# Optimization experiments

Hardware: AMD Instinct MI355X
Metric: run time of the kernel (lower is better)

Reference implementation:

```python
import jax, jax.numpy as jnp
import numpy as np

B_BOX, N_CLASS = 2, 20          # B, C from __init__
LAMBDA_C, LAMBDA_N = 5.0, 0.5   # self.lambda_c, self.lambda_n
GRID = 49                        # hard-coded 7x7 grid


def setup_inputs() -> dict:
    key = jax.random.key(0)
    k1, k2 = jax.random.split(key)
    outputs = jax.random.uniform(k1, (16384, GRID, 5 * B_BOX + N_CLASS), dtype=jnp.float32)
    target = jax.random.uniform(k2, (16384, 10, 5), dtype=jnp.float32)
    return {"outputs": outputs, "target": target}


def _forward(outputs, target):
    batch, n_obj = target.shape[0], target.shape[1]
    Bb = B_BOX
    # --- target preprocessing: sqrt(w,h), nan -> -1 ---
    tgt = target.at[:, :, 2:4].set(jnp.sqrt(target[:, :, 2:4]))
    tgt = jnp.nan_to_num(tgt, nan=-1.0)
    # --- grid-cell assignment (vectorized version of the batch*obj python loop) ---
    x, y = tgt[:, :, 0], tgt[:, :, 1]
    xi = jnp.trunc(7.0 * x).astype(jnp.int32)   # int(7*x) truncation semantics
    yi = jnp.trunc(7.0 * y).astype(jnp.int32)
    cell = jnp.clip(7 * yi + xi, 0, GRID - 1)
    valid = ((x != -1.0) & (xi >= 0)).astype(tgt.dtype)
    sel = jax.nn.one_hot(cell, GRID, dtype=tgt.dtype) * valid[..., None]   # [b,obj,49]
    ti = sel[:, :, :, None] * tgt[:, :, None, :]                           # [b,obj,49,5]
    ti = jnp.transpose(ti, (0, 2, 1, 3))                                   # [b,49,obj,5]
    # --- permute: move first Bb nonzero boxes of each cell to the top ---
    nonzero = jnp.sum(ti, axis=-1) > 0                                     # [b,49,obj]
    slot = jnp.cumsum(nonzero.astype(jnp.int32), axis=-1) - 1
    slot = jnp.where(nonzero, jnp.minimum(slot, Bb), Bb)                   # Bb = discard slot
    oh = jax.nn.one_hot(slot, Bb + 1, dtype=ti.dtype)                      # [b,49,obj,Bb+1]
    gt = jnp.einsum('bcos,bcod->bcsd', oh, ti)[:, :, :Bb]                  # [b,49,Bb,5]
    # --- iou_matrix (boxes stored as center +/- (sqrt_wh)^2 corners) ---
    pred5 = outputs[:, :, :5 * Bb].reshape(batch, GRID, Bb, 5)
    pdims = pred5[..., :4]
    pdims = pdims.at[..., 2:4].set(jnp.sqrt(pdims[..., 2:4]))
    gdims = gt[..., :4]
    gmin, gmax = gdims[..., :2] - gdims[..., 2:4] ** 2, gdims[..., :2] + gdims[..., 2:4] ** 2
    pmin, pmax = pdims[..., :2] - pdims[..., 2:4] ** 2, pdims[..., :2] + pdims[..., 2:4] ** 2
    # pairwise: axis2 = pred box, axis3 = gt box
    imin = jnp.maximum(gmin[:, :, None, :, :], pmin[:, :, :, None, :])
    imax = jnp.minimum(gmax[:, :, None, :, :], pmax[:, :, :, None, :])
    d = jnp.maximum(imax - imin, 0.0)
    inter = d[..., 0] * d[..., 1]                                          # [b,49,Bb,Bb]
    gwh, pwh = jnp.abs(gmax - gmin), jnp.abs(pmax - pmin)
    garea = (gwh[..., 0] * gwh[..., 1])[:, :, None, :]
    parea = (pwh[..., 0] * pwh[..., 1])[:, :, :, None]
    union = garea + parea - inter
    iou = jnp.where(union == 0, 0.0, inter / jnp.where(union == 0, 1.0, union))  # nan_to_num(i/u)
    t_index = jnp.argmax(iou, axis=2)                                      # [b,49,Bb]
    # --- construct_model_ground_truth: gather assigned gt box + truncated-int confidence ---
    idx = jnp.broadcast_to(t_index[..., None], gt.shape)
    gathered = jnp.take_along_axis(gt, idx, axis=2)                        # [b,49,Bb,5]
    r1wh, r2wh = pred5[..., 2:4] ** 2, gathered[..., 2:4] ** 2
    min1, max1 = pred5[..., :2] - 0.5 * r1wh, pred5[..., :2] + 0.5 * r1wh
    min2, max2 = gathered[..., :2] - 0.5 * r2wh, gathered[..., :2] + 0.5 * r2wh
    d2 = jnp.maximum(jnp.minimum(max1, max2) - jnp.maximum(min1, min2), 0.0)
    inter2 = d2[..., 0] * d2[..., 1]
    union2 = r1wh[..., 0] * r1wh[..., 1] + r2wh[..., 0] * r2wh[..., 1] - inter2
    conf = jnp.where((jnp.trunc(union2) == 0) | (jnp.trunc(inter2) == 0), 0.0,
                     jnp.trunc(inter2 / jnp.where(union2 == 0, 1.0, union2)))
    final_gt = gathered.at[..., 4].set(conf)
    # --- obj loss: lambda_c on x,y,w,h; 1.0 on confidence ---
    w = jnp.array([LAMBDA_C, LAMBDA_C, LAMBDA_C, LAMBDA_C, 1.0], dtype=outputs.dtype)
    obj_loss = jnp.sum(w * (final_gt - pred5) ** 2)
    # --- noobj loss (faithfully replicates original bug: mask is recreated per loop
    #     iteration, so only the last (batch, bbox) iteration's mask survives) ---
    pconf, gconf = pred5[..., 4], final_gt[..., 4]                         # [b,49,Bb]
    mask = jnp.ones_like(gconf)
    mask = mask.at[batch - 1, jnp.arange(GRID), t_index[batch - 1, :, Bb - 1]].set(0.0)
    noobj_loss = LAMBDA_N * jnp.sum(((pconf - gconf) * mask) ** 2)
    # --- class loss ---
    cls_scores = outputs[:, :, 5 * Bb:]                                    # [b,49,C]
    max_pred = jnp.max(cls_scores, axis=2)[..., None]                      # [b,49,1]
    pred_cls = jnp.argmax(cls_scores, axis=2)[..., None]                   # [b,49,1]
    predictions = max_pred * pconf                                         # [b,49,Bb]
    truths = (final_gt[..., 4] == pred_cls.astype(outputs.dtype)).astype(outputs.dtype)
    cell_mask = jnp.sign(jnp.sum(final_gt, axis=-1))                       # [b,49,Bb]
    class_loss = jnp.sum(cell_mask * (truths - predictions) ** 2)
    return (obj_loss + noobj_loss + class_loss) / batch


def reference(outputs, target):
    return _forward(outputs, target)
```

## Files before the change

### kernel.cpp

```cpp
#include <hip/hip_runtime.h>
#include <math.h>

#define GRID_CELLS 49
#define NOBJ 10
#define BB 2
#define NCLS 20
#define OUT_C 30
#define LAMBDA_C 5.0f
#define LAMBDA_N 0.5f
#define BLOCK 256

__global__ __launch_bounds__(BLOCK, 4) void yolo_loss_flat(
    const float* __restrict__ outputs,
    const float* __restrict__ target,
    float* __restrict__ out,
    int batch, float inv_batch)
{
    const int gid = blockIdx.x * BLOCK + threadIdx.x;
    float lsum = 0.0f;

    if (gid < batch * GRID_CELLS) {
        const int b = gid / GRID_CELLS;
        const int c = gid - b * GRID_CELLS;

        float g0[5] = {0.f, 0.f, 0.f, 0.f, 0.f};
        float g1[5] = {0.f, 0.f, 0.f, 0.f, 0.f};
        int cnt = 0;
        const float2* t2 = reinterpret_cast<const float2*>(target + (size_t)b * (NOBJ * 5));
        #pragma unroll
        for (int i = 0; i < 5; ++i) {
            float2 a0 = t2[5 * i + 0];
            float2 a1 = t2[5 * i + 1];
            float2 a2 = t2[5 * i + 2];
            float2 a3 = t2[5 * i + 3];
            float2 a4 = t2[5 * i + 4];
            float v[10] = {a0.x, a0.y, a1.x, a1.y, a2.x, a2.y, a3.x, a3.y, a4.x, a4.y};
            #pragma unroll
            for (int h = 0; h < 2; ++h) {
                float t0 = v[5 * h + 0];
                float t1 = v[5 * h + 1];
                float t2f = sqrtf(v[5 * h + 2]);
                float t3f = sqrtf(v[5 * h + 3]);
                float t4 = v[5 * h + 4];
                if (t0 != t0)  t0  = -1.0f;
                if (t1 != t1)  t1  = -1.0f;
                if (t2f != t2f) t2f = -1.0f;
                if (t3f != t3f) t3f = -1.0f;
                if (t4 != t4)  t4  = -1.0f;
                int xi = (int)truncf(7.0f * t0);
                int yi = (int)truncf(7.0f * t1);
                int cell = 7 * yi + xi;
                cell = cell < 0 ? 0 : (cell > GRID_CELLS - 1 ? GRID_CELLS - 1 : cell);
                bool valid = (t0 != -1.0f) && (xi >= 0);
                float s5 = t0 + t1 + t2f + t3f + t4;
                if (valid && (s5 > 0.0f) && cell == c) {
                    if (cnt == 0)      { g0[0]=t0; g0[1]=t1; g0[2]=t2f; g0[3]=t3f; g0[4]=t4; }
                    else if (cnt == 1) { g1[0]=t0; g1[1]=t1; g1[2]=t2f; g1[3]=t3f; g1[4]=t4; }
                    ++cnt;
                }
            }
        }
        float g[BB][5];
        #pragma unroll
        for (int d = 0; d < 5; ++d) { g[0][d] = g0[d]; g[1][d] = g1[d]; }

        const float2* r2 = reinterpret_cast<const float2*>(outputs + (size_t)gid * OUT_C);
        float pred[BB][5];
        {
            float2 p0 = r2[0], p1 = r2[1], p2 = r2[2], p3 = r2[3], p4 = r2[4];
            pred[0][0] = p0.x; pred[0][1] = p0.y; pred[0][2] = p1.x; pred[0][3] = p1.y; pred[0][4] = p2.x;
            pred[1][0] = p2.y; pred[1][1] = p3.x; pred[1][2] = p3.y; pred[1][3] = p4.x; pred[1][4] = p4.y;
        }
        float maxp; int cls;
        {
            float2 q0 = r2[5];
            maxp = q0.x; cls = 0;
            if (q0.y > maxp) { maxp = q0.y; cls = 1; }
            #pragma unroll
            for (int i = 1; i < NCLS / 2; ++i) {
                float2 q = r2[5 + i];
                if (q.x > maxp) { maxp = q.x; cls = 2 * i; }
                if (q.y > maxp) { maxp = q.y; cls = 2 * i + 1; }
            }
        }
        float fcls = (float)cls;

        float pminx[BB], pmaxx[BB], pminy[BB], pmaxy[BB], parea[BB];
        #pragma unroll
        for (int p = 0; p < BB; ++p) {
            float sw = sqrtf(pred[p][2]);
            float sh = sqrtf(pred[p][3]);
            float w2 = sw * sw, h2 = sh * sh;
            pminx[p] = pred[p][0] - w2; pmaxx[p] = pred[p][0] + w2;
            pminy[p] = pred[p][1] - h2; pmaxy[p] = pred[p][1] + h2;
            parea[p] = fabsf(pmaxx[p] - pminx[p]) * fabsf(pmaxy[p] - pminy[p]);
        }
        float gminx[BB], gmaxx[BB], gminy[BB], gmaxy[BB], garea[BB];
        #pragma unroll
        for (int s = 0; s < BB; ++s) {
            float w2 = g[s][2] * g[s][2], h2 = g[s][3] * g[s][3];
            gminx[s] = g[s][0] - w2; gmaxx[s] = g[s][0] + w2;
            gminy[s] = g[s][1] - h2; gmaxy[s] = g[s][1] + h2;
            garea[s] = fabsf(gmaxx[s] - gminx[s]) * fabsf(gmaxy[s] - gminy[s]);
        }
        int t_index[BB];
        #pragma unroll
        for (int s = 0; s < BB; ++s) {
            float best = 0.0f; int bi = 0;
            #pragma unroll
            for (int p = 0; p < BB; ++p) {
                float ix0 = fmaxf(gminx[s], pminx[p]);
                float iy0 = fmaxf(gminy[s], pminy[p]);
                float ix1 = fminf(gmaxx[s], pmaxx[p]);
                float iy1 = fminf(gmaxy[s], pmaxy[p]);
                float dx = fmaxf(ix1 - ix0, 0.0f);
                float dy = fmaxf(iy1 - iy0, 0.0f);
                float inter = dx * dy;
                float uni = garea[s] + parea[p] - inter;
                float iou = (uni == 0.0f) ? 0.0f : inter / uni;
                if (p == 0) { best = iou; bi = 0; }
                else if (iou > best) { best = iou; bi = p; }
            }
            t_index[s] = bi;
        }

        #pragma unroll
        for (int s = 0; s < BB; ++s) {
            float ga[5];
            #pragma unroll
            for (int d = 0; d < 5; ++d) ga[d] = (t_index[s] == 0) ? g[0][d] : g[1][d];
            float r1w = pred[s][2] * pred[s][2], r1h = pred[s][3] * pred[s][3];
            float r2w = ga[2] * ga[2],           r2h = ga[3] * ga[3];
            float min1x = pred[s][0] - 0.5f * r1w, max1x = pred[s][0] + 0.5f * r1w;
            float min1y = pred[s][1] - 0.5f * r1h, max1y = pred[s][1] + 0.5f * r1h;
            float min2x = ga[0] - 0.5f * r2w, max2x = ga[0] + 0.5f * r2w;
            float min2y = ga[1] - 0.5f * r2h, max2y = ga[1] + 0.5f * r2h;
            float dx = fmaxf(fminf(max1x, max2x) - fmaxf(min1x, min2x), 0.0f);
            float dy = fmaxf(fminf(max1y, max2y) - fmaxf(min1y, min2y), 0.0f);
            float inter2 = dx * dy;
            float uni2 = r1w * r1h + r2w * r2h - inter2;
            float conf;
            if (truncf(uni2) == 0.0f || truncf(inter2) == 0.0f) conf = 0.0f;
            else conf = truncf(inter2 / (uni2 == 0.0f ? 1.0f : uni2));
            #pragma unroll
            for (int d = 0; d < 4; ++d) {
                float df = ga[d] - pred[s][d];
                lsum += LAMBDA_C * df * df;
            }
            { float df = conf - pred[s][4]; lsum += df * df; }
            float m = 1.0f;
            if (b == batch - 1 && s == t_index[BB - 1]) m = 0.0f;
            float dn = (pred[s][4] - conf) * m;
            lsum += LAMBDA_N * dn * dn;
            float predn = maxp * pred[s][4];
            float truth = (conf == fcls) ? 1.0f : 0.0f;
            float sum5 = ga[0] + ga[1] + ga[2] + ga[3] + conf;
            float cm = (sum5 > 0.0f) ? 1.0f : ((sum5 < 0.0f) ? -1.0f : 0.0f);
            float dcl = truth - predn;
            lsum += cm * dcl * dcl;
        }
    }

    #pragma unroll
    for (int off = 32; off > 0; off >>= 1) lsum += __shfl_down(lsum, off, 64);
    __shared__ float red[BLOCK / 64];
    const int wid = threadIdx.x >> 6;
    const int lane = threadIdx.x & 63;
    if (lane == 0) red[wid] = lsum;
    __syncthreads();
    if (threadIdx.x == 0) {
        float s = 0.0f;
        #pragma unroll
        for (int w = 0; w < BLOCK / 64; ++w) s += red[w];
        atomicAdd(out, s * inv_batch);
    }
}

extern "C" void kernel_launch(void* const* d_in, const int* in_sizes, int n_in,
                              void* d_out, int out_size, void* d_ws, size_t ws_size,
                              hipStream_t stream) {
    const float* outputs = (const float*)d_in[0];
    const float* target  = (const float*)d_in[1];
    float* out = (float*)d_out;
    int batch = in_sizes[1] / (NOBJ * 5);
    int total = batch * GRID_CELLS;
    int nblocks = (total + BLOCK - 1) / BLOCK;
    hipMemsetAsync(out, 0, sizeof(float), stream);
    yolo_loss_flat<<<nblocks, BLOCK, 0, stream>>>(outputs, target, out, batch, 1.0f / (float)batch);
}
```

Measured before the change: 158.6 us.

## Scatter targets into shared-memory cell grid per block instead of per-thread scans

Each block now handles 5 whole batch items. Target objects are preprocessed once per object and scattered into a shared-memory per-cell ground-truth table, instead of every cell thread re-reading and re-testing all 10 targets. This removes redundant target loads and per-cell preprocessing. In exchange it adds two barriers, about 11KB of shared memory per block and a grid-wide zeroing pass. Only 245 of 256 threads do cell work, and the launch_bounds occupancy hint is dropped.

```diff
diff --git a/kernel.cpp b/kernel.cpp
--- a/kernel.cpp
+++ b/kernel.cpp
@@ -9,61 +9,84 @@
 #define LAMBDA_C 5.0f
 #define LAMBDA_N 0.5f
 #define BLOCK 256
-
-__global__ __launch_bounds__(BLOCK, 4) void yolo_loss_flat(
+#define ITEMS 5
+#define CELLW 11
+
+__global__ __launch_bounds__(BLOCK) void yolo_loss_shared(
     const float* __restrict__ outputs,
     const float* __restrict__ target,
     float* __restrict__ out,
     int batch, float inv_batch)
 {
-    const int gid = blockIdx.x * BLOCK + threadIdx.x;
+    __shared__ int   cellA[ITEMS][NOBJ];
+    __shared__ int   nzA[ITEMS][NOBJ];
+    __shared__ float tval[ITEMS][NOBJ][5];
+    __shared__ float gt[ITEMS][GRID_CELLS][CELLW];
+    __shared__ float red[BLOCK / 64];
+
+    const int t = threadIdx.x;
+    const int b0 = blockIdx.x * ITEMS;
+
+    for (int i = t; i < ITEMS * GRID_CELLS * CELLW; i += BLOCK)
+        (&gt[0][0][0])[i] = 0.0f;
+
+    if (t < ITEMS * NOBJ) {
+        const int li = t / NOBJ;
+        const int o  = t - li * NOBJ;
+        const int b  = b0 + li;
+        if (b < batch) {
+            const float* tp = target + (size_t)b * (NOBJ * 5) + o * 5;
+            float t0 = tp[0], t1 = tp[1];
+            float t2f = sqrtf(tp[2]), t3f = sqrtf(tp[3]);
+            float t4 = tp[4];
+            if (t0 != t0)   t0  = -1.0f;
+            if (t1 != t1)   t1  = -1.0f;
+            if (t2f != t2f) t2f = -1.0f;
+            if (t3f != t3f) t3f = -1.0f;
+            if (t4 != t4)   t4  = -1.0f;
+            int xi = (int)truncf(7.0f * t0);
+            int yi = (int)truncf(7.0f * t1);
+            int cell = 7 * yi + xi;
+            cell = cell < 0 ? 0 : (cell > GRID_CELLS - 1 ? GRID_CELLS - 1 : cell);
+            bool valid = (t0 != -1.0f) && (xi >= 0);
+            float s5 = t0 + t1 + t2f + t3f + t4;
+            cellA[li][o] = cell;
+            nzA[li][o] = (valid && (s5 > 0.0f)) ? 1 : 0;
+            tval[li][o][0] = t0; tval[li][o][1] = t1; tval[li][o][2] = t2f;
+            tval[li][o][3] = t3f; tval[li][o][4] = t4;
+        } else {
+            nzA[li][o] = 0;
+        }
+    }
+    __syncthreads();
+
+    if (t < ITEMS * NOBJ) {
+        const int li = t / NOBJ;
+        const int o  = t - li * NOBJ;
+        if (nzA[li][o]) {
+            const int c = cellA[li][o];
+            int slot = 0;
+            for (int p = 0; p < o; ++p) slot += (nzA[li][p] && cellA[li][p] == c) ? 1 : 0;
+            if (slot < BB) {
+                #pragma unroll
+                for (int d = 0; d < 5; ++d) gt[li][c][slot * 5 + d] = tval[li][o][d];
+            }
+        }
+    }
+    __syncthreads();
+
     float lsum = 0.0f;
-
-    if (gid < batch * GRID_CELLS) {
-        const int b = gid / GRID_CELLS;
-        const int c = gid - b * GRID_CELLS;
-
-        float g0[5] = {0.f, 0.f, 0.f, 0.f, 0.f};
-        float g1[5] = {0.f, 0.f, 0.f, 0.f, 0.f};
-        int cnt = 0;
-        const float2* t2 = reinterpret_cast<const float2*>(target + (size_t)b * (NOBJ * 5));
-        #pragma unroll
-        for (int i = 0; i < 5; ++i) {
-            float2 a0 = t2[5 * i + 0];
-            float2 a1 = t2[5 * i + 1];
-            float2 a2 = t2[5 * i + 2];
-            float2 a3 = t2[5 * i + 3];
-            float2 a4 = t2[5 * i + 4];
-            float v[10] = {a0.x, a0.y, a1.x, a1.y, a2.x, a2.y, a3.x, a3.y, a4.x, a4.y};
-            #pragma unroll
-            for (int h = 0; h < 2; ++h) {
-                float t0 = v[5 * h + 0];
-                float t1 = v[5 * h + 1];
-                float t2f = sqrtf(v[5 * h + 2]);
-                float t3f = sqrtf(v[5 * h + 3]);
-                float t4 = v[5 * h + 4];
-                if (t0 != t0)  t0  = -1.0f;
-                if (t1 != t1)  t1  = -1.0f;
-                if (t2f != t2f) t2f = -1.0f;
-                if (t3f != t3f) t3f = -1.0f;
-                if (t4 != t4)  t4  = -1.0f;
-                int xi = (int)truncf(7.0f * t0);
-                int yi = (int)truncf(7.0f * t1);
-                int cell = 7 * yi + xi;
-                cell = cell < 0 ? 0 : (cell > GRID_CELLS - 1 ? GRID_CELLS - 1 : cell);
-                bool valid = (t0 != -1.0f) && (xi >= 0);
-                float s5 = t0 + t1 + t2f + t3f + t4;
-                if (valid && (s5 > 0.0f) && cell == c) {
-                    if (cnt == 0)      { g0[0]=t0; g0[1]=t1; g0[2]=t2f; g0[3]=t3f; g0[4]=t4; }
-                    else if (cnt == 1) { g1[0]=t0; g1[1]=t1; g1[2]=t2f; g1[3]=t3f; g1[4]=t4; }
-                    ++cnt;
-                }
-            }
-        }
+    const int li = t / GRID_CELLS;
+    const int c  = t - li * GRID_CELLS;
+    const int b  = b0 + li;
+    if (t < ITEMS * GRID_CELLS && b < batch) {
         float g[BB][5];
         #pragma unroll
-        for (int d = 0; d < 5; ++d) { g[0][d] = g0[d]; g[1][d] = g1[d]; }
-
+        for (int s = 0; s < BB; ++s)
+            #pragma unroll
+            for (int d = 0; d < 5; ++d) g[s][d] = gt[li][c][s * 5 + d];
+
+        const int gid = b * GRID_CELLS + c;
         const float2* r2 = reinterpret_cast<const float2*>(outputs + (size_t)gid * OUT_C);
         float pred[BB][5];
         {
@@ -163,12 +186,11 @@
 
     #pragma unroll
     for (int off = 32; off > 0; off >>= 1) lsum += __shfl_down(lsum, off, 64);
-    __shared__ float red[BLOCK / 64];
-    const int wid = threadIdx.x >> 6;
-    const int lane = threadIdx.x & 63;
+    const int wid = t >> 6;
+    const int lane = t & 63;
     if (lane == 0) red[wid] = lsum;
     __syncthreads();
-    if (threadIdx.x == 0) {
+    if (t == 0) {
         float s = 0.0f;
         #pragma unroll
         for (int w = 0; w < BLOCK / 64; ++w) s += red[w];
@@ -183,8 +205,7 @@
     const float* target  = (const float*)d_in[1];
     float* out = (float*)d_out;
     int batch = in_sizes[1] / (NOBJ * 5);
-    int total = batch * GRID_CELLS;
-    int nblocks = (total + BLOCK - 1) / BLOCK;
+    int nblocks = (batch + ITEMS - 1) / ITEMS;
     hipMemsetAsync(out, 0, sizeof(float), stream);
-    yolo_loss_flat<<<nblocks, BLOCK, 0, stream>>>(outputs, target, out, batch, 1.0f / (float)batch);
+    yolo_loss_shared<<<nblocks, BLOCK, 0, stream>>>(outputs, target, out, batch, 1.0f / (float)batch);
 }
```

Measured after the change: 161.8 us. 2.0% more time.
